# Performance work log

Hardware: AMD Instinct MI355X
Metric: run time of the kernel (lower is better)

The kernel has to match this reference:

```python
import jax, jax.numpy as jnp
import numpy as np

NB_FEAT = 20000
NB_CLASSES = 30
N_EDGES = 640000
BATCH = 128


def setup_inputs() -> dict:
    key = jax.random.key(0)
    k1, k2, k3, k4, k5 = jax.random.split(key, 5)
    x = jax.random.normal(k1, (BATCH, NB_FEAT), dtype=jnp.float32)
    edge_index = jax.random.randint(k2, (2, N_EDGES), 0, NB_FEAT, dtype=jnp.int64)
    edge_weight = jax.random.uniform(k3, (N_EDGES,), dtype=jnp.float32)
    fc_w = jax.random.normal(k4, (NB_CLASSES, NB_FEAT), dtype=jnp.float32) * 0.01
    fc_b = jax.random.normal(k5, (NB_CLASSES,), dtype=jnp.float32) * 0.01
    return {"x": x, "edge_index": edge_index, "edge_weight": edge_weight,
            "fc_w": fc_w, "fc_b": fc_b}


def reference(x, edge_index, edge_weight, fc_w, fc_b):
    # SGConv(K=1, bias=False, lin.weight frozen to 1) == gcn_norm + one propagation.
    B, N = x.shape
    src, dst = edge_index[0], edge_index[1]
    # add self-loops with weight 1 (gcn_norm default fill_value=1)
    loop = jnp.arange(N)
    src_f = jnp.concatenate([src, loop])
    dst_f = jnp.concatenate([dst, loop])
    w_f = jnp.concatenate([edge_weight, jnp.ones((N,), edge_weight.dtype)])
    # symmetric normalization: deg over target index
    deg = jax.ops.segment_sum(w_f, dst_f, num_segments=N)  # (N,)
    dinv = jnp.where(deg > 0, jax.lax.rsqrt(deg), 0.0)
    wn = dinv[src_f] * w_f * dinv[dst_f]  # (E',)
    # batched gather-multiply-scatter; graph shared across batch, so vectorize over B
    msgs = x[:, src_f] * wn  # (B, E')
    diffused = jax.ops.segment_sum(msgs.T, dst_f, num_segments=N).T  # (B, N)
    # dropout p=0 -> no-op; dense FC + softmax
    logits = diffused @ fc_w.T + fc_b  # (B, C)
    return jax.nn.softmax(logits, axis=1)
```

## Files before the change

### kernel.cpp

```cpp
#include <hip/hip_runtime.h>


#define N_NODES   20000
#define N_EDGES_C 640000
#define N_CLASSES 30
#define CPAD      32

#define HBLKS     64
#define HNODES    10000
#define HEDGES    (N_EDGES_C / HBLKS)

#define BN        64
#define NBUCKET   313
#define NPB       (NBUCKET * BN)
#define NSLAB     256
#define SLAB_E    (N_EDGES_C / NSLAB)
#define NSCAN     (NBUCKET * NSLAB)
#define ECAP      2600

#define NCHUNK    64
#define NCHUNKS   313
#define XL_LD     130
#define GT_LD     68

#define FCB       ((NPB * CPAD) / 256)
#define DINVB     ((N_NODES + 255) / 256)

__global__ __launch_bounds__(256) void k1_hists(const int* __restrict__ src,
        const int* __restrict__ dst, const float* __restrict__ w,
        float* __restrict__ degp, int* __restrict__ cnt) {
    __shared__ float h[HNODES];
    int bid = blockIdx.x;
    if (bid < 2 * HBLKS) {
        int eb = bid >> 1, half = bid & 1;
        int nbase = half * HNODES;
        for (int i = threadIdx.x; i < HNODES; i += 256) h[i] = 0.f;
        __syncthreads();
        const int4* d4 = (const int4*)(dst + eb * HEDGES);
        const float4* w4 = (const float4*)(w + eb * HEDGES);
        for (int i = threadIdx.x; i < HEDGES / 4; i += 256) {
            int4 dv = d4[i]; float4 wv = w4[i];
            unsigned r;
            r = (unsigned)(dv.x - nbase); if (r < HNODES) atomicAdd(&h[r], wv.x);
            r = (unsigned)(dv.y - nbase); if (r < HNODES) atomicAdd(&h[r], wv.y);
            r = (unsigned)(dv.z - nbase); if (r < HNODES) atomicAdd(&h[r], wv.z);
            r = (unsigned)(dv.w - nbase); if (r < HNODES) atomicAdd(&h[r], wv.w);
        }
        __syncthreads();
        float* outp = degp + (size_t)bid * HNODES;
        for (int i = threadIdx.x; i < HNODES; i += 256) outp[i] = h[i];
    } else {
        int slab = bid - 2 * HBLKS;
        int* bc = (int*)h;
        for (int i = threadIdx.x; i < NBUCKET; i += 256) bc[i] = 0;
        __syncthreads();
        const int4* s4 = (const int4*)(src + slab * SLAB_E);
        for (int i = threadIdx.x; i < SLAB_E / 4; i += 256) {
            int4 v = s4[i];
            atomicAdd(&bc[v.x >> 6], 1);
            atomicAdd(&bc[v.y >> 6], 1);
            atomicAdd(&bc[v.z >> 6], 1);
            atomicAdd(&bc[v.w >> 6], 1);
        }
        __syncthreads();
        for (int b = threadIdx.x; b < NBUCKET; b += 256) cnt[b * NSLAB + slab] = bc[b];
    }
}

__global__ __launch_bounds__(256) void k2_prep(const int* __restrict__ cnt,
        int* __restrict__ btot, const float* __restrict__ fc_w,
        const float* __restrict__ degp, float* __restrict__ fc_wT,
        float* __restrict__ dinv) {
    int bid = blockIdx.x;
    if (bid < NBUCKET) {
        __shared__ int lds[256];
        int t = threadIdx.x;
        lds[t] = cnt[bid * NSLAB + t];
        __syncthreads();
        for (int o = 128; o > 0; o >>= 1) {
            if (t < o) lds[t] += lds[t + o];
            __syncthreads();
        }
        if (t == 0) btot[bid] = lds[0];
    } else if (bid < NBUCKET + FCB) {
        int idx = (bid - NBUCKET) * 256 + threadIdx.x;
        int n = idx >> 5, c = idx & 31;
        fc_wT[idx] = (c < N_CLASSES && n < N_NODES) ? fc_w[c * N_NODES + n] : 0.f;
    } else {
        int n = (bid - NBUCKET - FCB) * 256 + threadIdx.x;
        if (n < N_NODES) {
            int half = n / HNODES, nn = n - half * HNODES;
            float s = 1.0f;
            for (int eb = 0; eb < HBLKS; eb++)
                s += degp[(size_t)((eb << 1) | half) * HNODES + nn];
            dinv[n] = rsqrtf(s);
        }
    }
}

__global__ __launch_bounds__(256) void k3_off(const int* __restrict__ cnt,
        const int* __restrict__ btot, int* __restrict__ off) {
    __shared__ int lds[256];
    __shared__ int bb;
    int b = blockIdx.x, t = threadIdx.x;
    int s = 0;
    for (int i = t; i < b; i += 256) s += btot[i];
    lds[t] = s;
    __syncthreads();
    for (int o = 128; o > 0; o >>= 1) {
        if (t < o) lds[t] += lds[t + o];
        __syncthreads();
    }
    if (t == 0) bb = lds[0];
    __syncthreads();
    int base = bb;
    int v = cnt[b * NSLAB + t];
    lds[t] = v;
    __syncthreads();
    for (int o = 1; o < 256; o <<= 1) {
        int u = (t >= o) ? lds[t - o] : 0;
        __syncthreads();
        lds[t] += u;
        __syncthreads();
    }
    off[b * NSLAB + t] = base + lds[t] - v;
    if (b == NBUCKET - 1 && t == 255) off[NSCAN] = base + lds[t];
}

__global__ __launch_bounds__(512) void k4_scatter(const int* __restrict__ src,
        const int* __restrict__ dst, const float* __restrict__ w,
        const float* __restrict__ dinv, const int* __restrict__ off,
        int2* __restrict__ erec) {
    __shared__ int cur[NBUCKET];
    int slab = blockIdx.x;
    for (int b = threadIdx.x; b < NBUCKET; b += 512) cur[b] = off[b * NSLAB + slab];
    __syncthreads();
    int e0 = slab * SLAB_E;
    const int4* s4 = (const int4*)(src + e0);
    const int4* d4 = (const int4*)(dst + e0);
    const float4* w4 = (const float4*)(w + e0);
    for (int i = threadIdx.x; i < SLAB_E / 4; i += 512) {
        int4 sv = s4[i]; int4 dv = d4[i]; float4 wv = w4[i];
        int s, d, p; float wn;
        s = sv.x; d = dv.x; wn = dinv[s] * wv.x * dinv[d];
        p = atomicAdd(&cur[s >> 6], 1);
        erec[p] = make_int2(((s & 63) << 15) | d, __float_as_int(wn));
        s = sv.y; d = dv.y; wn = dinv[s] * wv.y * dinv[d];
        p = atomicAdd(&cur[s >> 6], 1);
        erec[p] = make_int2(((s & 63) << 15) | d, __float_as_int(wn));
        s = sv.z; d = dv.z; wn = dinv[s] * wv.z * dinv[d];
        p = atomicAdd(&cur[s >> 6], 1);
        erec[p] = make_int2(((s & 63) << 15) | d, __float_as_int(wn));
        s = sv.w; d = dv.w; wn = dinv[s] * wv.w * dinv[d];
        p = atomicAdd(&cur[s >> 6], 1);
        erec[p] = make_int2(((s & 63) << 15) | d, __float_as_int(wn));
    }
}

__global__ __launch_bounds__(512) void k5_fold(const int2* __restrict__ erec,
        const int* __restrict__ off, const float* __restrict__ dinv,
        const float* __restrict__ fc_wT, float* __restrict__ gT) {
    __shared__ int2 srt[ECAP];
    __shared__ int hist[BN];
    __shared__ int rowst[BN];
    __shared__ int cur[BN];
    int bucket = blockIdx.x;
    int nlo = bucket * BN;
    int bstart = off[bucket * NSLAB];
    int bend   = off[(bucket + 1) * NSLAB];
    int len = min(bend - bstart, ECAP);
    if (threadIdx.x < BN) hist[threadIdx.x] = 0;
    __syncthreads();
    for (int i = threadIdx.x; i < len; i += 512)
        atomicAdd(&hist[((unsigned)erec[bstart + i].x) >> 15], 1);
    __syncthreads();
    if (threadIdx.x < BN) {
        int h = hist[threadIdx.x];
        int v = h;
        #pragma unroll
        for (int o = 1; o < BN; o <<= 1) {
            int u = __shfl_up(v, o, 64);
            if (threadIdx.x >= o) v += u;
        }
        rowst[threadIdx.x] = v - h;
        cur[threadIdx.x]   = v - h;
    }
    __syncthreads();
    for (int i = threadIdx.x; i < len; i += 512) {
        int2 r = erec[bstart + i];
        int p = atomicAdd(&cur[((unsigned)r.x) >> 15], 1);
        srt[p] = r;
    }
    __syncthreads();
    int c = threadIdx.x & 31;
    int grp = threadIdx.x >> 5;
    for (int nn = grp; nn < BN; nn += 16) {
        int n = nlo + nn;
        if (n >= N_NODES) { gT[(size_t)n * CPAD + c] = 0.f; continue; }
        float di = dinv[n];
        float acc  = di * di * fc_wT[(size_t)n * CPAD + c];
        float acc2 = 0.f;
        int i = rowst[nn], re = i + hist[nn];
        for (; i + 1 < re; i += 2) {
            int2 r0 = srt[i], r1 = srt[i + 1];
            acc  += __int_as_float(r0.y) * fc_wT[(size_t)(r0.x & 0x7FFF) * CPAD + c];
            acc2 += __int_as_float(r1.y) * fc_wT[(size_t)(r1.x & 0x7FFF) * CPAD + c];
        }
        if (i < re) {
            int2 r0 = srt[i];
            acc += __int_as_float(r0.y) * fc_wT[(size_t)(r0.x & 0x7FFF) * CPAD + c];
        }
        gT[(size_t)n * CPAD + c] = acc + acc2;
    }
}

__global__ __launch_bounds__(512) void k6_gemm(const float* __restrict__ x,
        const float* __restrict__ gT, float* __restrict__ part) {
    __shared__ float xl[(NCHUNK / 2) * XL_LD];
    __shared__ float gt[CPAD * GT_LD];
    int ch = blockIdx.x, bh = blockIdx.y;
    int n0 = ch * NCHUNK;
    int b0 = bh * 64;
    for (int o = threadIdx.x; o < 64 * NCHUNK; o += 512) {
        int b = o >> 6, n = o & (NCHUNK - 1);
        int gn = n0 + n;
        float v = (gn < N_NODES) ? x[(size_t)(b0 + b) * N_NODES + gn] : 0.f;
        xl[(n >> 1) * XL_LD + b * 2 + (n & 1)] = v;
    }
    for (int o = threadIdx.x; o < NCHUNK * CPAD; o += 512) {
        int n = o >> 5, cc = o & 31;
        gt[cc * GT_LD + n] = gT[(size_t)n0 * CPAD + o];
    }
    __syncthreads();
    int wv = threadIdx.x >> 6, l = threadIdx.x & 63;
    float acc0 = 0.f, acc1 = 0.f, acc2 = 0.f, acc3 = 0.f;
    #pragma unroll
    for (int n4 = 0; n4 < NCHUNK / 4; n4++) {
        float2 xa = *(const float2*)&xl[(2 * n4) * XL_LD + l * 2];
        float2 xb = *(const float2*)&xl[(2 * n4 + 1) * XL_LD + l * 2];
        float4 ga = *(const float4*)&gt[(wv)      * GT_LD + 4 * n4];
        float4 gb = *(const float4*)&gt[(wv +  8) * GT_LD + 4 * n4];
        float4 gc = *(const float4*)&gt[(wv + 16) * GT_LD + 4 * n4];
        float4 gd = *(const float4*)&gt[(wv + 24) * GT_LD + 4 * n4];
        acc0 += xa.x * ga.x + xa.y * ga.y + xb.x * ga.z + xb.y * ga.w;
        acc1 += xa.x * gb.x + xa.y * gb.y + xb.x * gb.z + xb.y * gb.w;
        acc2 += xa.x * gc.x + xa.y * gc.y + xb.x * gc.z + xb.y * gc.w;
        acc3 += xa.x * gd.x + xa.y * gd.y + xb.x * gd.z + xb.y * gd.w;
    }
    size_t pb = (size_t)(ch * 2 + bh) * CPAD * 64;
    part[pb + (size_t)(wv)      * 64 + l] = acc0;
    part[pb + (size_t)(wv +  8) * 64 + l] = acc1;
    part[pb + (size_t)(wv + 16) * 64 + l] = acc2;
    part[pb + (size_t)(wv + 24) * 64 + l] = acc3;
}

__global__ __launch_bounds__(128) void k7_lred(const float* __restrict__ part,
        float* __restrict__ lpart) {
    int c = blockIdx.x, q = blockIdx.y;
    int b = threadIdx.x;
    int bhl = b >> 6, l = b & 63;
    float s = 0.f;
    for (int ch = q; ch < NCHUNKS; ch += 4)
        s += part[(((size_t)ch * 2 + bhl) * CPAD + c) * 64 + l];
    lpart[(q * N_CLASSES + c) * 128 + b] = s;
}

__global__ void k8_smax(const float* __restrict__ lpart,
        const float* __restrict__ fc_b, float* __restrict__ out) {
    int b = threadIdx.x;
    float v[N_CLASSES], m = -1e30f;
    #pragma unroll
    for (int c = 0; c < N_CLASSES; c++) {
        float s = fc_b[c];
        #pragma unroll
        for (int q = 0; q < 4; q++) s += lpart[(q * N_CLASSES + c) * 128 + b];
        v[c] = s; m = fmaxf(m, s);
    }
    float s = 0.f;
    #pragma unroll
    for (int c = 0; c < N_CLASSES; c++) { v[c] = __expf(v[c] - m); s += v[c]; }
    float inv = 1.0f / s;
    #pragma unroll
    for (int c = 0; c < N_CLASSES; c++) out[b * N_CLASSES + c] = v[c] * inv;
}

extern "C" void kernel_launch(void* const* d_in, const int* in_sizes, int n_in,
                              void* d_out, int out_size, void* d_ws, size_t ws_size,
                              hipStream_t stream) {
    const float* x          = (const float*)d_in[0];
    const int*   edge_index = (const int*)d_in[1];
    const float* ew         = (const float*)d_in[2];
    const float* fc_w       = (const float*)d_in[3];
    const float* fc_b       = (const float*)d_in[4];
    float* out = (float*)d_out;

    const int* src = edge_index;
    const int* dst = edge_index + N_EDGES_C;

    float* A     = (float*)d_ws;
    float* B     = A + 1282048;
    float* dinv  = B + 1280000;
    int*   cnt   = (int*)(dinv + N_NODES);
    int*   off   = cnt + NSCAN;
    int*   btot  = off + 80136;
    float* fc_wT = (float*)(btot + 320);
    float* gT    = fc_wT + (size_t)NPB * CPAD;
    float* lpart = gT + (size_t)NPB * CPAD;

    k1_hists<<<2 * HBLKS + NSLAB, 256, 0, stream>>>(src, dst, ew, A, cnt);
    k2_prep<<<NBUCKET + FCB + DINVB, 256, 0, stream>>>(cnt, btot, fc_w, A,
                                                       fc_wT, dinv);
    k3_off<<<NBUCKET, 256, 0, stream>>>(cnt, btot, off);
    k4_scatter<<<NSLAB, 512, 0, stream>>>(src, dst, ew, dinv, off, (int2*)B);
    k5_fold<<<NBUCKET, 512, 0, stream>>>((int2*)B, off, dinv, fc_wT, gT);
    k6_gemm<<<dim3(NCHUNKS, 2), 512, 0, stream>>>(x, gT, A);
    k7_lred<<<dim3(N_CLASSES, 4), 128, 0, stream>>>(A, lpart);
    k8_smax<<<1, 128, 0, stream>>>(lpart, fc_b, out);
}
```

Before: 101.2 us.

## Fuse prep kernels, fold normalization into fc_wT, and merge final reductions

Merges the bucket-total and offset-scan kernels into the prep kernel by computing each bucket's prefix directly from the raw counts. The degree reduction now uses a 32-lane shuffle alongside the fc_w transpose, and dinv[src] is pre-multiplied into fc_wT, so the scatter kernel no longer gathers dinv per edge. dinv[dst] is applied once per node in the fold kernel. The GEMM runs over 128 chunk-groups of three chunks each, and the partial-sum reduction and softmax are fused into one final kernel, cutting the launch count from eight to six. The cost is redundant prefix summation of cnt in every bucket block and a serial 128-step loop in the final kernel.

```diff
diff --git a/kernel.cpp b/kernel.cpp
--- a/kernel.cpp
+++ b/kernel.cpp
@@ -22,9 +22,9 @@
 #define NCHUNKS   313
 #define XL_LD     130
 #define GT_LD     68
+#define GBX       128
 
 #define FCB       ((NPB * CPAD) / 256)
-#define DINVB     ((N_NODES + 255) / 256)
 
 __global__ __launch_bounds__(256) void k1_hists(const int* __restrict__ src,
         const int* __restrict__ dst, const float* __restrict__ w,
@@ -68,69 +68,59 @@
 }
 
 __global__ __launch_bounds__(256) void k2_prep(const int* __restrict__ cnt,
-        int* __restrict__ btot, const float* __restrict__ fc_w,
+        int* __restrict__ off, const float* __restrict__ fc_w,
         const float* __restrict__ degp, float* __restrict__ fc_wT,
         float* __restrict__ dinv) {
     int bid = blockIdx.x;
+    int t = threadIdx.x;
     if (bid < NBUCKET) {
         __shared__ int lds[256];
-        int t = threadIdx.x;
-        lds[t] = cnt[bid * NSLAB + t];
+        __shared__ int bb;
+        int b = bid;
+        int s = 0;
+        int lim = b * NSLAB;
+        for (int i = t; i < lim; i += 256) s += cnt[i];
+        lds[t] = s;
         __syncthreads();
         for (int o = 128; o > 0; o >>= 1) {
             if (t < o) lds[t] += lds[t + o];
             __syncthreads();
         }
-        if (t == 0) btot[bid] = lds[0];
-    } else if (bid < NBUCKET + FCB) {
-        int idx = (bid - NBUCKET) * 256 + threadIdx.x;
+        if (t == 0) bb = lds[0];
+        __syncthreads();
+        int base = bb;
+        int v = cnt[b * NSLAB + t];
+        lds[t] = v;
+        __syncthreads();
+        for (int o = 1; o < 256; o <<= 1) {
+            int u = (t >= o) ? lds[t - o] : 0;
+            __syncthreads();
+            lds[t] += u;
+            __syncthreads();
+        }
+        off[b * NSLAB + t] = base + lds[t] - v;
+        if (b == NBUCKET - 1 && t == 255) off[NSCAN] = base + lds[t];
+    } else {
+        int idx = (bid - NBUCKET) * 256 + t;
         int n = idx >> 5, c = idx & 31;
-        fc_wT[idx] = (c < N_CLASSES && n < N_NODES) ? fc_w[c * N_NODES + n] : 0.f;
-    } else {
-        int n = (bid - NBUCKET - FCB) * 256 + threadIdx.x;
+        float v = 0.f;
         if (n < N_NODES) {
             int half = n / HNODES, nn = n - half * HNODES;
-            float s = 1.0f;
-            for (int eb = 0; eb < HBLKS; eb++)
-                s += degp[(size_t)((eb << 1) | half) * HNODES + nn];
-            dinv[n] = rsqrtf(s);
-        }
-    }
-}
-
-__global__ __launch_bounds__(256) void k3_off(const int* __restrict__ cnt,
-        const int* __restrict__ btot, int* __restrict__ off) {
-    __shared__ int lds[256];
-    __shared__ int bb;
-    int b = blockIdx.x, t = threadIdx.x;
-    int s = 0;
-    for (int i = t; i < b; i += 256) s += btot[i];
-    lds[t] = s;
-    __syncthreads();
-    for (int o = 128; o > 0; o >>= 1) {
-        if (t < o) lds[t] += lds[t + o];
-        __syncthreads();
-    }
-    if (t == 0) bb = lds[0];
-    __syncthreads();
-    int base = bb;
-    int v = cnt[b * NSLAB + t];
-    lds[t] = v;
-    __syncthreads();
-    for (int o = 1; o < 256; o <<= 1) {
-        int u = (t >= o) ? lds[t - o] : 0;
-        __syncthreads();
-        lds[t] += u;
-        __syncthreads();
-    }
-    off[b * NSLAB + t] = base + lds[t] - v;
-    if (b == NBUCKET - 1 && t == 255) off[NSCAN] = base + lds[t];
-}
-
-__global__ __launch_bounds__(512) void k4_scatter(const int* __restrict__ src,
+            v = degp[(size_t)((c << 1) | half) * HNODES + nn]
+              + degp[(size_t)(((c + 32) << 1) | half) * HNODES + nn];
+        }
+        #pragma unroll
+        for (int m = 16; m > 0; m >>= 1) v += __shfl_xor(v, m, 32);
+        float di = rsqrtf(v + 1.0f);
+        if (n < N_NODES && c == 0) dinv[n] = di;
+        float fw = (n < N_NODES && c < N_CLASSES) ? fc_w[c * N_NODES + n] : 0.f;
+        fc_wT[idx] = di * fw;
+    }
+}
+
+__global__ __launch_bounds__(512) void k3_scatter(const int* __restrict__ src,
         const int* __restrict__ dst, const float* __restrict__ w,
-        const float* __restrict__ dinv, const int* __restrict__ off,
-        int2* __restrict__ erec) {
+        const int* __restrict__ off, int2* __restrict__ erec) {
     __shared__ int cur[NBUCKET];
     int slab = blockIdx.x;
     for (int b = threadIdx.x; b < NBUCKET; b += 512) cur[b] = off[b * NSLAB + slab];
@@ -141,23 +131,19 @@
     const float4* w4 = (const float4*)(w + e0);
     for (int i = threadIdx.x; i < SLAB_E / 4; i += 512) {
         int4 sv = s4[i]; int4 dv = d4[i]; float4 wv = w4[i];
-        int s, d, p; float wn;
-        s = sv.x; d = dv.x; wn = dinv[s] * wv.x * dinv[d];
-        p = atomicAdd(&cur[s >> 6], 1);
-        erec[p] = make_int2(((s & 63) << 15) | d, __float_as_int(wn));
-        s = sv.y; d = dv.y; wn = dinv[s] * wv.y * dinv[d];
-        p = atomicAdd(&cur[s >> 6], 1);
-        erec[p] = make_int2(((s & 63) << 15) | d, __float_as_int(wn));
-        s = sv.z; d = dv.z; wn = dinv[s] * wv.z * dinv[d];
-        p = atomicAdd(&cur[s >> 6], 1);
-        erec[p] = make_int2(((s & 63) << 15) | d, __float_as_int(wn));
-        s = sv.w; d = dv.w; wn = dinv[s] * wv.w * dinv[d];
-        p = atomicAdd(&cur[s >> 6], 1);
-        erec[p] = make_int2(((s & 63) << 15) | d, __float_as_int(wn));
-    }
-}
-
-__global__ __launch_bounds__(512) void k5_fold(const int2* __restrict__ erec,
+        int s, p;
+        s = sv.x; p = atomicAdd(&cur[s >> 6], 1);
+        erec[p] = make_int2(((s & 63) << 15) | dv.x, __float_as_int(wv.x));
+        s = sv.y; p = atomicAdd(&cur[s >> 6], 1);
+        erec[p] = make_int2(((s & 63) << 15) | dv.y, __float_as_int(wv.y));
+        s = sv.z; p = atomicAdd(&cur[s >> 6], 1);
+        erec[p] = make_int2(((s & 63) << 15) | dv.z, __float_as_int(wv.z));
+        s = sv.w; p = atomicAdd(&cur[s >> 6], 1);
+        erec[p] = make_int2(((s & 63) << 15) | dv.w, __float_as_int(wv.w));
+    }
+}
+
+__global__ __launch_bounds__(512) void k4_fold(const int2* __restrict__ erec,
         const int* __restrict__ off, const float* __restrict__ dinv,
         const float* __restrict__ fc_wT, float* __restrict__ gT) {
     __shared__ int2 srt[ECAP];
@@ -196,9 +182,11 @@
     int grp = threadIdx.x >> 5;
     for (int nn = grp; nn < BN; nn += 16) {
         int n = nlo + nn;
-        if (n >= N_NODES) { gT[(size_t)n * CPAD + c] = 0.f; continue; }
-        float di = dinv[n];
-        float acc  = di * di * fc_wT[(size_t)n * CPAD + c];
+        if (n >= N_NODES) {
+            if (n < NPB) gT[(size_t)n * CPAD + c] = 0.f;
+            continue;
+        }
+        float acc  = fc_wT[(size_t)n * CPAD + c];
         float acc2 = 0.f;
         int i = rowst[nn], re = i + hist[nn];
         for (; i + 1 < re; i += 2) {
@@ -210,78 +198,85 @@
             int2 r0 = srt[i];
             acc += __int_as_float(r0.y) * fc_wT[(size_t)(r0.x & 0x7FFF) * CPAD + c];
         }
-        gT[(size_t)n * CPAD + c] = acc + acc2;
-    }
-}
-
-__global__ __launch_bounds__(512) void k6_gemm(const float* __restrict__ x,
+        gT[(size_t)n * CPAD + c] = dinv[n] * (acc + acc2);
+    }
+}
+
+__global__ __launch_bounds__(512) void k5_gemm(const float* __restrict__ x,
         const float* __restrict__ gT, float* __restrict__ part) {
     __shared__ float xl[(NCHUNK / 2) * XL_LD];
     __shared__ float gt[CPAD * GT_LD];
-    int ch = blockIdx.x, bh = blockIdx.y;
-    int n0 = ch * NCHUNK;
+    int bx = blockIdx.x, bh = blockIdx.y;
     int b0 = bh * 64;
-    for (int o = threadIdx.x; o < 64 * NCHUNK; o += 512) {
-        int b = o >> 6, n = o & (NCHUNK - 1);
-        int gn = n0 + n;
-        float v = (gn < N_NODES) ? x[(size_t)(b0 + b) * N_NODES + gn] : 0.f;
-        xl[(n >> 1) * XL_LD + b * 2 + (n & 1)] = v;
-    }
-    for (int o = threadIdx.x; o < NCHUNK * CPAD; o += 512) {
-        int n = o >> 5, cc = o & 31;
-        gt[cc * GT_LD + n] = gT[(size_t)n0 * CPAD + o];
-    }
-    __syncthreads();
     int wv = threadIdx.x >> 6, l = threadIdx.x & 63;
     float acc0 = 0.f, acc1 = 0.f, acc2 = 0.f, acc3 = 0.f;
-    #pragma unroll
-    for (int n4 = 0; n4 < NCHUNK / 4; n4++) {
-        float2 xa = *(const float2*)&xl[(2 * n4) * XL_LD + l * 2];
-        float2 xb = *(const float2*)&xl[(2 * n4 + 1) * XL_LD + l * 2];
-        float4 ga = *(const float4*)&gt[(wv)      * GT_LD + 4 * n4];
-        float4 gb = *(const float4*)&gt[(wv +  8) * GT_LD + 4 * n4];
-        float4 gc = *(const float4*)&gt[(wv + 16) * GT_LD + 4 * n4];
-        float4 gd = *(const float4*)&gt[(wv + 24) * GT_LD + 4 * n4];
-        acc0 += xa.x * ga.x + xa.y * ga.y + xb.x * ga.z + xb.y * ga.w;
-        acc1 += xa.x * gb.x + xa.y * gb.y + xb.x * gb.z + xb.y * gb.w;
-        acc2 += xa.x * gc.x + xa.y * gc.y + xb.x * gc.z + xb.y * gc.w;
-        acc3 += xa.x * gd.x + xa.y * gd.y + xb.x * gd.z + xb.y * gd.w;
-    }
-    size_t pb = (size_t)(ch * 2 + bh) * CPAD * 64;
+    for (int j = 0; j < 3; j++) {
+        int ch = bx + GBX * j;
+        if (ch >= NCHUNKS) break;
+        int n0 = ch * NCHUNK;
+        for (int o = threadIdx.x; o < 64 * NCHUNK; o += 512) {
+            int b = o >> 6, n = o & (NCHUNK - 1);
+            int gn = n0 + n;
+            float v = (gn < N_NODES) ? x[(size_t)(b0 + b) * N_NODES + gn] : 0.f;
+            xl[(n >> 1) * XL_LD + b * 2 + (n & 1)] = v;
+        }
+        for (int o = threadIdx.x; o < NCHUNK * CPAD; o += 512) {
+            int n = o >> 5, cc = o & 31;
+            gt[cc * GT_LD + n] = gT[(size_t)n0 * CPAD + o];
+        }
+        __syncthreads();
+        #pragma unroll
+        for (int n4 = 0; n4 < NCHUNK / 4; n4++) {
+            float2 xa = *(const float2*)&xl[(2 * n4) * XL_LD + l * 2];
+            float2 xb = *(const float2*)&xl[(2 * n4 + 1) * XL_LD + l * 2];
+            float4 ga = *(const float4*)&gt[(wv)      * GT_LD + 4 * n4];
+            float4 gb = *(const float4*)&gt[(wv +  8) * GT_LD + 4 * n4];
+            float4 gc = *(const float4*)&gt[(wv + 16) * GT_LD + 4 * n4];
+            float4 gd = *(const float4*)&gt[(wv + 24) * GT_LD + 4 * n4];
+            acc0 += xa.x * ga.x + xa.y * ga.y + xb.x * ga.z + xb.y * ga.w;
+            acc1 += xa.x * gb.x + xa.y * gb.y + xb.x * gb.z + xb.y * gb.w;
+            acc2 += xa.x * gc.x + xa.y * gc.y + xb.x * gc.z + xb.y * gc.w;
+            acc3 += xa.x * gd.x + xa.y * gd.y + xb.x * gd.z + xb.y * gd.w;
+        }
+        __syncthreads();
+    }
+    size_t pb = (size_t)(bx * 2 + bh) * CPAD * 64;
     part[pb + (size_t)(wv)      * 64 + l] = acc0;
     part[pb + (size_t)(wv +  8) * 64 + l] = acc1;
     part[pb + (size_t)(wv + 16) * 64 + l] = acc2;
     part[pb + (size_t)(wv + 24) * 64 + l] = acc3;
 }
 
-__global__ __launch_bounds__(128) void k7_lred(const float* __restrict__ part,
-        float* __restrict__ lpart) {
-    int c = blockIdx.x, q = blockIdx.y;
-    int b = threadIdx.x;
-    int bhl = b >> 6, l = b & 63;
-    float s = 0.f;
-    for (int ch = q; ch < NCHUNKS; ch += 4)
-        s += part[(((size_t)ch * 2 + bhl) * CPAD + c) * 64 + l];
-    lpart[(q * N_CLASSES + c) * 128 + b] = s;
-}
-
-__global__ void k8_smax(const float* __restrict__ lpart,
+__global__ __launch_bounds__(1024) void k6_final(const float* __restrict__ part,
         const float* __restrict__ fc_b, float* __restrict__ out) {
-    int b = threadIdx.x;
-    float v[N_CLASSES], m = -1e30f;
-    #pragma unroll
-    for (int c = 0; c < N_CLASSES; c++) {
-        float s = fc_b[c];
-        #pragma unroll
-        for (int q = 0; q < 4; q++) s += lpart[(q * N_CLASSES + c) * 128 + b];
-        v[c] = s; m = fmaxf(m, s);
-    }
-    float s = 0.f;
-    #pragma unroll
-    for (int c = 0; c < N_CLASSES; c++) { v[c] = __expf(v[c] - m); s += v[c]; }
-    float inv = 1.0f / s;
-    #pragma unroll
-    for (int c = 0; c < N_CLASSES; c++) out[b * N_CLASSES + c] = v[c] * inv;
+    __shared__ float lg[64 * 33];
+    int bh = blockIdx.x;
+    int l = threadIdx.x & 63;
+    int cq = threadIdx.x >> 6;
+    float s0 = 0.f, s1 = 0.f;
+    for (int bx = 0; bx < GBX; bx++) {
+        const float* p = part + (size_t)(bx * 2 + bh) * CPAD * 64;
+        s0 += p[cq * 64 + l];
+        s1 += p[(cq + 16) * 64 + l];
+    }
+    lg[l * 33 + cq]      = s0 + ((cq < N_CLASSES) ? fc_b[cq] : 0.f);
+    lg[l * 33 + cq + 16] = s1 + ((cq + 16 < N_CLASSES) ? fc_b[cq + 16] : 0.f);
+    __syncthreads();
+    if (threadIdx.x < 64) {
+        int b = bh * 64 + threadIdx.x;
+        float v[N_CLASSES], m = -1e30f;
+        #pragma unroll
+        for (int c = 0; c < N_CLASSES; c++) {
+            v[c] = lg[threadIdx.x * 33 + c];
+            m = fmaxf(m, v[c]);
+        }
+        float s = 0.f;
+        #pragma unroll
+        for (int c = 0; c < N_CLASSES; c++) { v[c] = __expf(v[c] - m); s += v[c]; }
+        float inv = 1.0f / s;
+        #pragma unroll
+        for (int c = 0; c < N_CLASSES; c++) out[b * N_CLASSES + c] = v[c] * inv;
+    }
 }
 
 extern "C" void kernel_launch(void* const* d_in, const int* in_sizes, int n_in,
@@ -298,22 +293,17 @@
     const int* dst = edge_index + N_EDGES_C;
 
     float* A     = (float*)d_ws;
-    float* B     = A + 1282048;
+    float* B     = A + 1280000;
     float* dinv  = B + 1280000;
     int*   cnt   = (int*)(dinv + N_NODES);
     int*   off   = cnt + NSCAN;
-    int*   btot  = off + 80136;
-    float* fc_wT = (float*)(btot + 320);
+    float* fc_wT = (float*)(off + 80136);
     float* gT    = fc_wT + (size_t)NPB * CPAD;
-    float* lpart = gT + (size_t)NPB * CPAD;
 
     k1_hists<<<2 * HBLKS + NSLAB, 256, 0, stream>>>(src, dst, ew, A, cnt);
-    k2_prep<<<NBUCKET + FCB + DINVB, 256, 0, stream>>>(cnt, btot, fc_w, A,
-                                                       fc_wT, dinv);
-    k3_off<<<NBUCKET, 256, 0, stream>>>(cnt, btot, off);
-    k4_scatter<<<NSLAB, 512, 0, stream>>>(src, dst, ew, dinv, off, (int2*)B);
-    k5_fold<<<NBUCKET, 512, 0, stream>>>((int2*)B, off, dinv, fc_wT, gT);
-    k6_gemm<<<dim3(NCHUNKS, 2), 512, 0, stream>>>(x, gT, A);
-    k7_lred<<<dim3(N_CLASSES, 4), 128, 0, stream>>>(A, lpart);
-    k8_smax<<<1, 128, 0, stream>>>(lpart, fc_b, out);
-}
+    k2_prep<<<NBUCKET + FCB, 256, 0, stream>>>(cnt, off, fc_w, A, fc_wT, dinv);
+    k3_scatter<<<NSLAB, 512, 0, stream>>>(src, dst, ew, off, (int2*)B);
+    k4_fold<<<NBUCKET, 512, 0, stream>>>((int2*)B, off, dinv, fc_wT, gT);
+    k5_gemm<<<dim3(GBX, 2), 512, 0, stream>>>(x, gT, A);
+    k6_final<<<2, 1024, 0, stream>>>(A, fc_b, out);
+}
```

Result: slower. 126.0 us (+24.4%).

## Stage fc_w transpose through LDS, accumulate chunks per GEMM block, fuse reduction with softmax

Applied to the files above, without the earlier changes.

The fc_w transpose now goes through a shared-memory tile, so both the global reads and the global writes are coalesced. The GEMM kernel now uses 128 blocks per batch half, and each block loops over up to three node chunks while keeping its accumulators in registers, which shrinks the partial-sum buffer. The separate cross-chunk reduction and softmax kernels are merged into one two-block kernel, removing a launch and the intermediate lpart buffer. In exchange the GEMM runs with fewer blocks and the final reduction is serial over 128 partials per thread.

```diff
diff --git a/kernel.cpp b/kernel.cpp
--- a/kernel.cpp
+++ b/kernel.cpp
@@ -22,8 +22,8 @@
 #define NCHUNKS   313
 #define XL_LD     130
 #define GT_LD     68
-
-#define FCB       ((NPB * CPAD) / 256)
+#define GBX       128
+
 #define DINVB     ((N_NODES + 255) / 256)
 
 __global__ __launch_bounds__(256) void k1_hists(const int* __restrict__ src,
@@ -72,9 +72,9 @@
         const float* __restrict__ degp, float* __restrict__ fc_wT,
         float* __restrict__ dinv) {
     int bid = blockIdx.x;
+    int t = threadIdx.x;
     if (bid < NBUCKET) {
         __shared__ int lds[256];
-        int t = threadIdx.x;
         lds[t] = cnt[bid * NSLAB + t];
         __syncthreads();
         for (int o = 128; o > 0; o >>= 1) {
@@ -82,12 +82,24 @@
             __syncthreads();
         }
         if (t == 0) btot[bid] = lds[0];
-    } else if (bid < NBUCKET + FCB) {
-        int idx = (bid - NBUCKET) * 256 + threadIdx.x;
-        int n = idx >> 5, c = idx & 31;
-        fc_wT[idx] = (c < N_CLASSES && n < N_NODES) ? fc_w[c * N_NODES + n] : 0.f;
+    } else if (bid < 2 * NBUCKET) {
+        __shared__ float tile[CPAD][65];
+        int n0 = (bid - NBUCKET) * 64;
+        #pragma unroll
+        for (int k = 0; k < 8; k++) {
+            int c = k * 4 + (t >> 6), nn = t & 63;
+            int n = n0 + nn;
+            tile[c][nn] = (c < N_CLASSES && n < N_NODES) ? fc_w[c * N_NODES + n] : 0.f;
+        }
+        __syncthreads();
+        #pragma unroll
+        for (int k = 0; k < 8; k++) {
+            int idx = k * 256 + t;
+            int nn = idx >> 5, c = idx & 31;
+            fc_wT[(size_t)(n0 + nn) * CPAD + c] = tile[c][nn];
+        }
     } else {
-        int n = (bid - NBUCKET - FCB) * 256 + threadIdx.x;
+        int n = (bid - 2 * NBUCKET) * 256 + t;
         if (n < N_NODES) {
             int half = n / HNODES, nn = n - half * HNODES;
             float s = 1.0f;
@@ -196,7 +208,10 @@
     int grp = threadIdx.x >> 5;
     for (int nn = grp; nn < BN; nn += 16) {
         int n = nlo + nn;
-        if (n >= N_NODES) { gT[(size_t)n * CPAD + c] = 0.f; continue; }
+        if (n >= N_NODES) {
+            if (n < NPB) gT[(size_t)n * CPAD + c] = 0.f;
+            continue;
+        }
         float di = dinv[n];
         float acc  = di * di * fc_wT[(size_t)n * CPAD + c];
         float acc2 = 0.f;
@@ -218,70 +233,77 @@
         const float* __restrict__ gT, float* __restrict__ part) {
     __shared__ float xl[(NCHUNK / 2) * XL_LD];
     __shared__ float gt[CPAD * GT_LD];
-    int ch = blockIdx.x, bh = blockIdx.y;
-    int n0 = ch * NCHUNK;
+    int bx = blockIdx.x, bh = blockIdx.y;
     int b0 = bh * 64;
-    for (int o = threadIdx.x; o < 64 * NCHUNK; o += 512) {
-        int b = o >> 6, n = o & (NCHUNK - 1);
-        int gn = n0 + n;
-        float v = (gn < N_NODES) ? x[(size_t)(b0 + b) * N_NODES + gn] : 0.f;
-        xl[(n >> 1) * XL_LD + b * 2 + (n & 1)] = v;
-    }
-    for (int o = threadIdx.x; o < NCHUNK * CPAD; o += 512) {
-        int n = o >> 5, cc = o & 31;
-        gt[cc * GT_LD + n] = gT[(size_t)n0 * CPAD + o];
-    }
-    __syncthreads();
     int wv = threadIdx.x >> 6, l = threadIdx.x & 63;
     float acc0 = 0.f, acc1 = 0.f, acc2 = 0.f, acc3 = 0.f;
-    #pragma unroll
-    for (int n4 = 0; n4 < NCHUNK / 4; n4++) {
-        float2 xa = *(const float2*)&xl[(2 * n4) * XL_LD + l * 2];
-        float2 xb = *(const float2*)&xl[(2 * n4 + 1) * XL_LD + l * 2];
-        float4 ga = *(const float4*)&gt[(wv)      * GT_LD + 4 * n4];
-        float4 gb = *(const float4*)&gt[(wv +  8) * GT_LD + 4 * n4];
-        float4 gc = *(const float4*)&gt[(wv + 16) * GT_LD + 4 * n4];
-        float4 gd = *(const float4*)&gt[(wv + 24) * GT_LD + 4 * n4];
-        acc0 += xa.x * ga.x + xa.y * ga.y + xb.x * ga.z + xb.y * ga.w;
-        acc1 += xa.x * gb.x + xa.y * gb.y + xb.x * gb.z + xb.y * gb.w;
-        acc2 += xa.x * gc.x + xa.y * gc.y + xb.x * gc.z + xb.y * gc.w;
-        acc3 += xa.x * gd.x + xa.y * gd.y + xb.x * gd.z + xb.y * gd.w;
-    }
-    size_t pb = (size_t)(ch * 2 + bh) * CPAD * 64;
+    for (int j = 0; j < 3; j++) {
+        int ch = bx + GBX * j;
+        if (ch >= NCHUNKS) break;
+        int n0 = ch * NCHUNK;
+        for (int o = threadIdx.x; o < 64 * NCHUNK; o += 512) {
+            int b = o >> 6, n = o & (NCHUNK - 1);
+            int gn = n0 + n;
+            float v = (gn < N_NODES) ? x[(size_t)(b0 + b) * N_NODES + gn] : 0.f;
+            xl[(n >> 1) * XL_LD + b * 2 + (n & 1)] = v;
+        }
+        for (int o = threadIdx.x; o < NCHUNK * CPAD; o += 512) {
+            int n = o >> 5, cc = o & 31;
+            gt[cc * GT_LD + n] = gT[(size_t)n0 * CPAD + o];
+        }
+        __syncthreads();
+        #pragma unroll
+        for (int n4 = 0; n4 < NCHUNK / 4; n4++) {
+            float2 xa = *(const float2*)&xl[(2 * n4) * XL_LD + l * 2];
+            float2 xb = *(const float2*)&xl[(2 * n4 + 1) * XL_LD + l * 2];
+            float4 ga = *(const float4*)&gt[(wv)      * GT_LD + 4 * n4];
+            float4 gb = *(const float4*)&gt[(wv +  8) * GT_LD + 4 * n4];
+            float4 gc = *(const float4*)&gt[(wv + 16) * GT_LD + 4 * n4];
+            float4 gd = *(const float4*)&gt[(wv + 24) * GT_LD + 4 * n4];
+            acc0 += xa.x * ga.x + xa.y * ga.y + xb.x * ga.z + xb.y * ga.w;
+            acc1 += xa.x * gb.x + xa.y * gb.y + xb.x * gb.z + xb.y * gb.w;
+            acc2 += xa.x * gc.x + xa.y * gc.y + xb.x * gc.z + xb.y * gc.w;
+            acc3 += xa.x * gd.x + xa.y * gd.y + xb.x * gd.z + xb.y * gd.w;
+        }
+        __syncthreads();
+    }
+    size_t pb = (size_t)(bx * 2 + bh) * CPAD * 64;
     part[pb + (size_t)(wv)      * 64 + l] = acc0;
     part[pb + (size_t)(wv +  8) * 64 + l] = acc1;
     part[pb + (size_t)(wv + 16) * 64 + l] = acc2;
     part[pb + (size_t)(wv + 24) * 64 + l] = acc3;
 }
 
-__global__ __launch_bounds__(128) void k7_lred(const float* __restrict__ part,
-        float* __restrict__ lpart) {
-    int c = blockIdx.x, q = blockIdx.y;
-    int b = threadIdx.x;
-    int bhl = b >> 6, l = b & 63;
-    float s = 0.f;
-    for (int ch = q; ch < NCHUNKS; ch += 4)
-        s += part[(((size_t)ch * 2 + bhl) * CPAD + c) * 64 + l];
-    lpart[(q * N_CLASSES + c) * 128 + b] = s;
-}
-
-__global__ void k8_smax(const float* __restrict__ lpart,
+__global__ __launch_bounds__(1024) void k7_final(const float* __restrict__ part,
         const float* __restrict__ fc_b, float* __restrict__ out) {
-    int b = threadIdx.x;
-    float v[N_CLASSES], m = -1e30f;
-    #pragma unroll
-    for (int c = 0; c < N_CLASSES; c++) {
-        float s = fc_b[c];
-        #pragma unroll
-        for (int q = 0; q < 4; q++) s += lpart[(q * N_CLASSES + c) * 128 + b];
-        v[c] = s; m = fmaxf(m, s);
-    }
-    float s = 0.f;
-    #pragma unroll
-    for (int c = 0; c < N_CLASSES; c++) { v[c] = __expf(v[c] - m); s += v[c]; }
-    float inv = 1.0f / s;
-    #pragma unroll
-    for (int c = 0; c < N_CLASSES; c++) out[b * N_CLASSES + c] = v[c] * inv;
+    __shared__ float lg[64 * 33];
+    int bh = blockIdx.x;
+    int l = threadIdx.x & 63;
+    int cq = threadIdx.x >> 6;
+    float s0 = 0.f, s1 = 0.f;
+    for (int bx = 0; bx < GBX; bx++) {
+        const float* p = part + (size_t)(bx * 2 + bh) * CPAD * 64;
+        s0 += p[cq * 64 + l];
+        s1 += p[(cq + 16) * 64 + l];
+    }
+    lg[l * 33 + cq]      = s0 + ((cq < N_CLASSES) ? fc_b[cq] : 0.f);
+    lg[l * 33 + cq + 16] = s1 + ((cq + 16 < N_CLASSES) ? fc_b[cq + 16] : 0.f);
+    __syncthreads();
+    if (threadIdx.x < 64) {
+        int b = bh * 64 + threadIdx.x;
+        float v[N_CLASSES], m = -1e30f;
+        #pragma unroll
+        for (int c = 0; c < N_CLASSES; c++) {
+            v[c] = lg[threadIdx.x * 33 + c];
+            m = fmaxf(m, v[c]);
+        }
+        float s = 0.f;
+        #pragma unroll
+        for (int c = 0; c < N_CLASSES; c++) { v[c] = __expf(v[c] - m); s += v[c]; }
+        float inv = 1.0f / s;
+        #pragma unroll
+        for (int c = 0; c < N_CLASSES; c++) out[b * N_CLASSES + c] = v[c] * inv;
+    }
 }
 
 extern "C" void kernel_launch(void* const* d_in, const int* in_sizes, int n_in,
@@ -298,22 +320,20 @@
     const int* dst = edge_index + N_EDGES_C;
 
     float* A     = (float*)d_ws;
-    float* B     = A + 1282048;
+    float* B     = A + 1280000;
     float* dinv  = B + 1280000;
     int*   cnt   = (int*)(dinv + N_NODES);
     int*   off   = cnt + NSCAN;
     int*   btot  = off + 80136;
     float* fc_wT = (float*)(btot + 320);
     float* gT    = fc_wT + (size_t)NPB * CPAD;
-    float* lpart = gT + (size_t)NPB * CPAD;
 
     k1_hists<<<2 * HBLKS + NSLAB, 256, 0, stream>>>(src, dst, ew, A, cnt);
-    k2_prep<<<NBUCKET + FCB + DINVB, 256, 0, stream>>>(cnt, btot, fc_w, A,
-                                                       fc_wT, dinv);
+    k2_prep<<<2 * NBUCKET + DINVB, 256, 0, stream>>>(cnt, btot, fc_w, A,
+                                                     fc_wT, dinv);
     k3_off<<<NBUCKET, 256, 0, stream>>>(cnt, btot, off);
     k4_scatter<<<NSLAB, 512, 0, stream>>>(src, dst, ew, dinv, off, (int2*)B);
     k5_fold<<<NBUCKET, 512, 0, stream>>>((int2*)B, off, dinv, fc_wT, gT);
-    k6_gemm<<<dim3(NCHUNKS, 2), 512, 0, stream>>>(x, gT, A);
-    k7_lred<<<dim3(N_CLASSES, 4), 128, 0, stream>>>(A, lpart);
-    k8_smax<<<1, 128, 0, stream>>>(lpart, fc_b, out);
-}
+    k6_gemm<<<dim3(GBX, 2), 512, 0, stream>>>(x, gT, A);
+    k7_final<<<2, 1024, 0, stream>>>(A, fc_b, out);
+}
```

Result: faster. 92.33 us (-8.8%).
